# Performance work log

Hardware: AMD Instinct MI355X
Metric: run time of the kernel (lower is better)

## Reference

```python
import jax, jax.numpy as jnp
import numpy as np

EPS = 1e-6  # ieps_ln_default

def layernorm(x, g, b, ndims):
    # LayerNorm over the last `ndims` dims (matches nn.LayerNorm(normalized_shape))
    ax = tuple(range(x.ndim - ndims, x.ndim))
    m = jnp.mean(x, ax, keepdims=True)
    v = jnp.var(x, ax, keepdims=True)
    return (x - m) * jax.lax.rsqrt(v + EPS) * g + b

def setup_inputs() -> dict:
    key = jax.random.key(0)
    ks = jax.random.split(key, 9)
    B, S, H, D = 4, 2048, 8, 128   # bsize, seql, num_head, head_dim (isize=1024)
    FH = 512                        # _head_fhsize = 4*isize // num_head
    sc = 0.02
    return {
        "heads_input": jax.random.normal(ks[0], (B, S, H, D), jnp.float32),
        # trans_ifg: GroupLinear(2*hsize -> 2*hsize) per head
        "W_ifg": jax.random.normal(ks[1], (H, 2 * D, 2 * D), jnp.float32) * sc,
        "b_ifg": jnp.zeros((H, 2 * D), jnp.float32),
        # trans_hid: GroupLinear(2*hsize -> fhsize), LN, ReLU, GroupLinear(fhsize -> hsize)
        "W_hid1": jax.random.normal(ks[2], (H, 2 * D, FH), jnp.float32) * sc,
        "b_hid1": jnp.zeros((H, FH), jnp.float32),
        "hid_g": jnp.ones((H, FH), jnp.float32),
        "hid_b": jnp.zeros((H, FH), jnp.float32),
        "W_hid2": jax.random.normal(ks[3], (H, FH, D), jnp.float32) * sc,
        "b_hid2": jnp.zeros((H, D), jnp.float32),
        # trans_og: GroupLinear(2*hsize -> hsize) + LN
        "W_og": jax.random.normal(ks[4], (H, 2 * D, D), jnp.float32) * sc,
        "b_og": jnp.zeros((H, D), jnp.float32),
        "og_g": jnp.ones((H, D), jnp.float32),
        "og_b": jnp.zeros((H, D), jnp.float32),
        # normer_csum LN((H, D)); normer_ifg LN((H, 2, D))
        "csum_g": jnp.ones((H, D), jnp.float32),
        "csum_b": jnp.zeros((H, D), jnp.float32),
        "ifg_g": jnp.ones((H, 2, D), jnp.float32),
        "ifg_b": jnp.zeros((H, 2, D), jnp.float32),
        "init_cx": jnp.zeros((1, H, D), jnp.float32),
    }

def reference(heads_input, W_ifg, b_ifg, W_hid1, b_hid1, hid_g, hid_b,
              W_hid2, b_hid2, W_og, b_og, og_g, og_b,
              csum_g, csum_b, ifg_g, ifg_b, init_cx):
    B, S, H, D = heads_input.shape
    # normer_csum(cumsum of right-shifted input)
    shifted = jnp.concatenate([jnp.zeros((B, 1, H, D), heads_input.dtype),
                               heads_input[:, :-1]], axis=1)
    csum = layernorm(jnp.cumsum(shifted, axis=1), csum_g, csum_b, 2)
    gh = jnp.concatenate([heads_input, csum], axis=-1)  # (B,S,H,2D)
    # input/forget gates: per-head GroupLinear then LN over (H,2,D)
    ifg = jnp.einsum('bshi,hio->bsho', gh, W_ifg) + b_ifg
    ifg = layernorm(ifg.reshape(B, S, H, 2, D), ifg_g, ifg_b, 3)
    igate, fgate = ifg[..., 0, :], ifg[..., 1, :]
    # hidden: GroupLinear -> LN -> ReLU -> GroupLinear
    hid = jnp.einsum('bshi,hio->bsho', gh, W_hid1) + b_hid1
    hid = jax.nn.relu(layernorm(hid, hid_g, hid_b, 2))
    hidden = jnp.einsum('bshi,hio->bsho', hid, W_hid2) + b_hid2
    fgate = jax.nn.sigmoid(fgate)
    igh = jax.nn.sigmoid(igate) * hidden
    # LGateFunc: cell_t = fgate_t * cell_{t-1} + igh_t, cell_0 from init_cx
    c0 = jnp.broadcast_to(init_cx, (B, H, D)).astype(heads_input.dtype)
    def step(c, x):
        f, i = x
        c = f * c + i
        return c, c
    _, cells = jax.lax.scan(step, c0, (jnp.moveaxis(fgate, 1, 0), jnp.moveaxis(igh, 1, 0)))
    cell = jnp.moveaxis(cells, 0, 1)  # (B,S,H,D)
    # output gate
    og = jnp.einsum('bshi,hio->bsho', jnp.concatenate([heads_input, cell], axis=-1), W_og) + b_og
    og = layernorm(og, og_g, og_b, 2)
    return jax.nn.sigmoid(og) * cell
```

## Files before the change

### kernel.cpp

```cpp
#include <hip/hip_runtime.h>
#include <hip/hip_bf16.h>

#define DEV static __device__ __forceinline__

constexpr int B = 4, S = 2048, H = 8, D = 128, FH = 512;
constexpr int M = B * S;
constexpr int SC = 64;
constexpr int NCH = S / SC;

typedef __attribute__((ext_vector_type(8))) short short8;
typedef __attribute__((ext_vector_type(4))) float f32x4;

DEV float sigmoidf_(float x) { return 1.0f / (1.0f + __expf(-x)); }
DEV float b2f(unsigned short u) { union { unsigned int i; float f; } x; x.i = (unsigned int)u << 16; return x.f; }
DEV unsigned short f2bu(float f) { __hip_bfloat16 b = __float2bfloat16(f); union { __hip_bfloat16 b; unsigned short u; } x; x.b = b; return x.u; }

__global__ void k_wcvt(const float* __restrict__ W, __hip_bfloat16* __restrict__ Wt,
                       int K, int N) {
  __shared__ float t[32][33];
  int h = blockIdx.z;
  int k0 = blockIdx.x * 32, n0 = blockIdx.y * 32;
  int tx = threadIdx.x, ty = threadIdx.y;
  #pragma unroll
  for (int r = 0; r < 32; r += 8)
    t[ty + r][tx] = W[((size_t)h * K + k0 + ty + r) * N + n0 + tx];
  __syncthreads();
  #pragma unroll
  for (int r = 0; r < 32; r += 8)
    Wt[((size_t)h * N + n0 + ty + r) * K + k0 + tx] = __float2bfloat16(t[tx][ty + r]);
}

__global__ void k_pre1(const float* __restrict__ x, float* __restrict__ chsum) {
  int bh = blockIdx.x, ch = blockIdx.y, d = threadIdx.x;
  int b = bh >> 3, h = bh & 7;
  size_t base = ((size_t)(b * S + ch * SC) * H + h) * D + d;
  float s = 0.0f;
  for (int i = 0; i < SC; ++i) s += x[base + (size_t)i * H * D];
  chsum[((size_t)bh * NCH + ch) * D + d] = s;
}

__global__ void k_pre2(const float* __restrict__ chsum, float* __restrict__ choff) {
  int bh = blockIdx.x, d = threadIdx.x;
  float a = 0.0f;
  for (int c = 0; c < NCH; ++c) {
    size_t idx = ((size_t)bh * NCH + c) * D + d;
    choff[idx] = a;
    a += chsum[idx];
  }
}

__global__ void k_pre3(const float* __restrict__ x, const float* __restrict__ choff,
                       __hip_bfloat16* __restrict__ P) {
  int bh = blockIdx.x, ch = blockIdx.y, d = threadIdx.x;
  int b = bh >> 3, h = bh & 7;
  float acc = choff[((size_t)bh * NCH + ch) * D + d];
  for (int i = 0; i < SC; ++i) {
    size_t mh = ((size_t)b * S + ch * SC + i) * H + h;
    P[mh * D + d] = __float2bfloat16(acc);
    acc += x[mh * D + d];
  }
}

DEV void block_stats(float lsum, float lss, int n, float& mean, float& var) {
  #pragma unroll
  for (int o = 32; o > 0; o >>= 1) {
    lsum += __shfl_down(lsum, o);
    lss  += __shfl_down(lss, o);
  }
  __shared__ float wsum[4], wss[4];
  int wid = threadIdx.x >> 6;
  if ((threadIdx.x & 63) == 0) { wsum[wid] = lsum; wss[wid] = lss; }
  __syncthreads();
  float s = 0.0f, q = 0.0f;
  #pragma unroll
  for (int i = 0; i < 4; ++i) { s += wsum[i]; q += wss[i]; }
  mean = s / n;
  var = q / n - mean * mean;
}

__global__ __launch_bounds__(256) void k_csum_ln(const __hip_bfloat16* __restrict__ P,
                                                 const float* __restrict__ g,
                                                 const float* __restrict__ bb,
                                                 __hip_bfloat16* __restrict__ csum) {
  size_t m = blockIdx.x;
  int t = threadIdx.x;
  ushort4 raw = ((const ushort4*)(P + m * 1024))[t];
  float v0 = b2f(raw.x), v1 = b2f(raw.y), v2 = b2f(raw.z), v3 = b2f(raw.w);
  float lsum = v0 + v1 + v2 + v3;
  float lss = v0 * v0 + v1 * v1 + v2 * v2 + v3 * v3;
  float mean, var;
  block_stats(lsum, lss, 1024, mean, var);
  float rs = rsqrtf(var + 1e-6f);
  float4 gv = *(const float4*)(g + t * 4);
  float4 bv = *(const float4*)(bb + t * 4);
  ushort4 o;
  o.x = f2bu((v0 - mean) * rs * gv.x + bv.x);
  o.y = f2bu((v1 - mean) * rs * gv.y + bv.y);
  o.z = f2bu((v2 - mean) * rs * gv.z + bv.z);
  o.w = f2bu((v3 - mean) * rs * gv.w + bv.w);
  ((ushort4*)((unsigned short*)csum + m * 1024))[t] = o;
}

template <int N, int K, int AKIND, int EPI>
__global__ __launch_bounds__(512) void k_mgemm(
    const __hip_bfloat16* __restrict__ Ab,
    const float* __restrict__ Af0, const float* __restrict__ Af1,
    const __hip_bfloat16* __restrict__ Wt, const float* __restrict__ bias,
    float* __restrict__ out_f, __hip_bfloat16* __restrict__ out_b,
    float* __restrict__ ifg) {
  constexpr int BM = 256, BN = 128, BK = 32;
  constexpr int LDA = 40;
  __shared__ __align__(16) short As[BM * LDA];
  __shared__ __align__(16) short Bs[BN * LDA];
  int h = blockIdx.z;
  int m0 = blockIdx.y * BM, n0 = blockIdx.x * BN;
  int tid = threadIdx.x;
  int w = tid >> 6, lane = tid & 63;
  int wr = w >> 1, wc = w & 1;
  int l15 = lane & 15, l4 = lane >> 4;
  f32x4 acc[4][4] = {};
  for (int kt = 0; kt < K; kt += BK) {
    #pragma unroll
    for (int r = 0; r < 2; ++r) {
      int q = tid + r * 512;
      int row = q >> 2, cq = q & 3;
      int kk = kt + cq * 8;
      short8 v;
      if (AKIND == 0) {
        v = *reinterpret_cast<const short8*>(Ab + ((size_t)(m0 + row) * H + h) * K + kk);
      } else if (AKIND == 2 && kk >= D) {
        v = *reinterpret_cast<const short8*>(Ab + ((size_t)(m0 + row) * H + h) * D + (kk - D));
      } else {
        const float* src;
        if (AKIND == 1 && kk >= D) src = Af1 + ((size_t)(m0 + row) * H + h) * D + (kk - D);
        else                       src = Af0 + ((size_t)(m0 + row) * H + h) * D + kk;
        float4 f0 = ((const float4*)src)[0];
        float4 f1 = ((const float4*)src)[1];
        short8 t;
        t[0] = (short)f2bu(f0.x); t[1] = (short)f2bu(f0.y);
        t[2] = (short)f2bu(f0.z); t[3] = (short)f2bu(f0.w);
        t[4] = (short)f2bu(f1.x); t[5] = (short)f2bu(f1.y);
        t[6] = (short)f2bu(f1.z); t[7] = (short)f2bu(f1.w);
        v = t;
      }
      *reinterpret_cast<short8*>(As + row * LDA + cq * 8) = v;
    }
    {
      int row = tid >> 2, cq = tid & 3;
      short8 v = *reinterpret_cast<const short8*>(
          Wt + ((size_t)h * N + n0 + row) * K + kt + cq * 8);
      *reinterpret_cast<short8*>(Bs + row * LDA + cq * 8) = v;
    }
    __syncthreads();
    short8 a[4], bfr[4];
    #pragma unroll
    for (int i = 0; i < 4; ++i)
      a[i] = *reinterpret_cast<const short8*>(As + (wr * 64 + i * 16 + l15) * LDA + l4 * 8);
    #pragma unroll
    for (int j = 0; j < 4; ++j)
      bfr[j] = *reinterpret_cast<const short8*>(Bs + (wc * 64 + j * 16 + l15) * LDA + l4 * 8);
    #pragma unroll
    for (int i = 0; i < 4; ++i)
      #pragma unroll
      for (int j = 0; j < 4; ++j)
        acc[i][j] = __builtin_amdgcn_mfma_f32_16x16x32_bf16(a[i], bfr[j], acc[i][j], 0, 0, 0);
    __syncthreads();
  }
  #pragma unroll
  for (int i = 0; i < 4; ++i) {
    #pragma unroll
    for (int j = 0; j < 4; ++j) {
      #pragma unroll
      for (int r = 0; r < 4; ++r) {
        int mg = m0 + wr * 64 + i * 16 + l4 * 4 + r;
        int o = n0 + wc * 64 + j * 16 + l15;
        float v = acc[i][j][r] + bias[h * N + o];
        size_t mh = (size_t)mg * H + h;
        if (EPI == 0) {
          out_f[mh * N + o] = v;
        } else if (EPI == 1) {
          out_b[mh * N + o] = __float2bfloat16(v);
        } else {
          size_t idx = mh * 256 + o;
          ifg[idx] = ifg[idx] * v;
        }
      }
    }
  }
}

__global__ __launch_bounds__(256) void k_ifg_ln(float* __restrict__ ifg,
                                                const float* __restrict__ g,
                                                const float* __restrict__ bb) {
  size_t m = blockIdx.x;
  float* row = ifg + m * 2048;
  int t = threadIdx.x;
  float4 v0 = ((const float4*)row)[t];
  float4 v1 = ((const float4*)row)[t + 256];
  float lsum = v0.x + v0.y + v0.z + v0.w + v1.x + v1.y + v1.z + v1.w;
  float lss = v0.x * v0.x + v0.y * v0.y + v0.z * v0.z + v0.w * v0.w +
              v1.x * v1.x + v1.y * v1.y + v1.z * v1.z + v1.w * v1.w;
  float mean, var;
  block_stats(lsum, lss, 2048, mean, var);
  float rs = rsqrtf(var + 1e-6f);
  float4 g0 = ((const float4*)g)[t], g1 = ((const float4*)g)[t + 256];
  float4 b0 = ((const float4*)bb)[t], b1 = ((const float4*)bb)[t + 256];
  float4 o0, o1;
  o0.x = sigmoidf_((v0.x - mean) * rs * g0.x + b0.x);
  o0.y = sigmoidf_((v0.y - mean) * rs * g0.y + b0.y);
  o0.z = sigmoidf_((v0.z - mean) * rs * g0.z + b0.z);
  o0.w = sigmoidf_((v0.w - mean) * rs * g0.w + b0.w);
  o1.x = sigmoidf_((v1.x - mean) * rs * g1.x + b1.x);
  o1.y = sigmoidf_((v1.y - mean) * rs * g1.y + b1.y);
  o1.z = sigmoidf_((v1.z - mean) * rs * g1.z + b1.z);
  o1.w = sigmoidf_((v1.w - mean) * rs * g1.w + b1.w);
  ((float4*)row)[t] = o0;
  ((float4*)row)[t + 256] = o1;
}

__global__ __launch_bounds__(256) void k_hid_ln(__hip_bfloat16* __restrict__ hid,
                                                const float* __restrict__ g,
                                                const float* __restrict__ bb) {
  size_t m = blockIdx.x;
  unsigned short* row = (unsigned short*)(hid + m * 4096);
  int t = threadIdx.x;
  short8 r0 = ((const short8*)row)[t * 2];
  short8 r1 = ((const short8*)row)[t * 2 + 1];
  float v[16];
  float lsum = 0.0f, lss = 0.0f;
  #pragma unroll
  for (int i = 0; i < 8; ++i) {
    v[i] = b2f((unsigned short)r0[i]);
    v[i + 8] = b2f((unsigned short)r1[i]);
  }
  #pragma unroll
  for (int i = 0; i < 16; ++i) { lsum += v[i]; lss += v[i] * v[i]; }
  float mean, var;
  block_stats(lsum, lss, 4096, mean, var);
  float rs = rsqrtf(var + 1e-6f);
  short8 o0, o1;
  #pragma unroll
  for (int i = 0; i < 16; ++i) {
    int j = t * 16 + i;
    float o = (v[i] - mean) * rs * g[j] + bb[j];
    o = o > 0.0f ? o : 0.0f;
    if (i < 8) o0[i] = (short)f2bu(o); else o1[i - 8] = (short)f2bu(o);
  }
  ((short8*)row)[t * 2] = o0;
  ((short8*)row)[t * 2 + 1] = o1;
}

__global__ void k_scan1(const float* __restrict__ ifg, float* __restrict__ chF,
                        float* __restrict__ chI) {
  int bh = blockIdx.x, ch = blockIdx.y, d = threadIdx.x;
  int b = bh >> 3, h = bh & 7;
  float F = 1.0f, I = 0.0f;
  for (int i = 0; i < SC; ++i) {
    size_t mh = ((size_t)b * S + ch * SC + i) * H + h;
    float iv = ifg[mh * 256 + d];
    float fv = ifg[mh * 256 + 128 + d];
    F *= fv;
    I = fv * I + iv;
  }
  size_t idx = ((size_t)bh * NCH + ch) * D + d;
  chF[idx] = F;
  chI[idx] = I;
}

__global__ void k_scan2(const float* __restrict__ chF, const float* __restrict__ chI,
                        const float* __restrict__ init_cx, float* __restrict__ cst) {
  int bh = blockIdx.x, d = threadIdx.x;
  int h = bh & 7;
  float c = init_cx[h * D + d];
  for (int ch = 0; ch < NCH; ++ch) {
    size_t idx = ((size_t)bh * NCH + ch) * D + d;
    cst[idx] = c;
    c = chF[idx] * c + chI[idx];
  }
}

__global__ void k_scan3(const float* __restrict__ ifg, const float* __restrict__ cst,
                        float* __restrict__ cell) {
  int bh = blockIdx.x, ch = blockIdx.y, d = threadIdx.x;
  int b = bh >> 3, h = bh & 7;
  float c = cst[((size_t)bh * NCH + ch) * D + d];
  for (int i = 0; i < SC; ++i) {
    size_t mh = ((size_t)b * S + ch * SC + i) * H + h;
    c = ifg[mh * 256 + 128 + d] * c + ifg[mh * 256 + d];
    cell[mh * D + d] = c;
  }
}

__global__ __launch_bounds__(256) void k_og_out(const float* __restrict__ og,
                                                const float* __restrict__ cell,
                                                const float* __restrict__ g,
                                                const float* __restrict__ bb,
                                                float* __restrict__ out) {
  size_t m = blockIdx.x;
  const float* row = og + m * 1024;
  int t = threadIdx.x;
  float4 v = ((const float4*)row)[t];
  float lsum = v.x + v.y + v.z + v.w;
  float lss = v.x * v.x + v.y * v.y + v.z * v.z + v.w * v.w;
  float mean, var;
  block_stats(lsum, lss, 1024, mean, var);
  float rs = rsqrtf(var + 1e-6f);
  float4 gv = ((const float4*)g)[t];
  float4 bv = ((const float4*)bb)[t];
  float4 cv = ((const float4*)(cell + m * 1024))[t];
  float4 o;
  o.x = sigmoidf_((v.x - mean) * rs * gv.x + bv.x) * cv.x;
  o.y = sigmoidf_((v.y - mean) * rs * gv.y + bv.y) * cv.y;
  o.z = sigmoidf_((v.z - mean) * rs * gv.z + bv.z) * cv.z;
  o.w = sigmoidf_((v.w - mean) * rs * gv.w + bv.w) * cv.w;
  ((float4*)(out + m * 1024))[t] = o;
}

extern "C" void kernel_launch(void* const* d_in, const int* in_sizes, int n_in,
                              void* d_out, int out_size, void* d_ws, size_t ws_size,
                              hipStream_t stream) {
  (void)in_sizes; (void)n_in; (void)out_size; (void)ws_size;
  const float* x       = (const float*)d_in[0];
  const float* W_ifg   = (const float*)d_in[1];
  const float* b_ifg   = (const float*)d_in[2];
  const float* W_hid1  = (const float*)d_in[3];
  const float* b_hid1  = (const float*)d_in[4];
  const float* hid_g   = (const float*)d_in[5];
  const float* hid_b   = (const float*)d_in[6];
  const float* W_hid2  = (const float*)d_in[7];
  const float* b_hid2  = (const float*)d_in[8];
  const float* W_og    = (const float*)d_in[9];
  const float* b_og    = (const float*)d_in[10];
  const float* og_g    = (const float*)d_in[11];
  const float* og_b    = (const float*)d_in[12];
  const float* csum_g  = (const float*)d_in[13];
  const float* csum_b  = (const float*)d_in[14];
  const float* ifg_g   = (const float*)d_in[15];
  const float* ifg_b   = (const float*)d_in[16];
  const float* init_cx = (const float*)d_in[17];
  float* out = (float*)d_out;

  char* w = (char*)d_ws;
  __hip_bfloat16* Pb     = (__hip_bfloat16*)w;
  float* ifg             = (float*)w;
  float* og              = (float*)w;
  __hip_bfloat16* hid    = (__hip_bfloat16*)(w + 67108864);
  float* cell            = (float*)(w + 67108864);
  __hip_bfloat16* csum   = (__hip_bfloat16*)(w + 134217728);
  __hip_bfloat16* wt_ifg = (__hip_bfloat16*)(w + 150994944);
  __hip_bfloat16* wt_h1  = (__hip_bfloat16*)(w + 152043520);
  __hip_bfloat16* wt_h2  = (__hip_bfloat16*)(w + 154140672);
  __hip_bfloat16* wt_og  = (__hip_bfloat16*)(w + 155189248);
  float* chsum           = (float*)(w + 155713536);
  float* choff           = (float*)(w + 156237824);
  float* chF             = (float*)(w + 156762112);
  float* chI             = (float*)(w + 157286400);
  float* cst             = (float*)(w + 157810688);

  k_wcvt<<<dim3(8, 8, 8),  dim3(32, 8), 0, stream>>>(W_ifg,  wt_ifg, 256, 256);
  k_wcvt<<<dim3(8, 16, 8), dim3(32, 8), 0, stream>>>(W_hid1, wt_h1,  256, 512);
  k_wcvt<<<dim3(16, 4, 8), dim3(32, 8), 0, stream>>>(W_hid2, wt_h2,  512, 128);
  k_wcvt<<<dim3(8, 4, 8),  dim3(32, 8), 0, stream>>>(W_og,   wt_og,  256, 128);

  k_pre1<<<dim3(32, NCH), dim3(D), 0, stream>>>(x, chsum);
  k_pre2<<<dim3(32), dim3(D), 0, stream>>>(chsum, choff);
  k_pre3<<<dim3(32, NCH), dim3(D), 0, stream>>>(x, choff, Pb);
  k_csum_ln<<<dim3(M), dim3(256), 0, stream>>>(Pb, csum_g, csum_b, csum);

  k_mgemm<256, 256, 2, 0><<<dim3(2, 32, 8), dim3(512), 0, stream>>>(
      csum, x, nullptr, wt_ifg, b_ifg, ifg, nullptr, nullptr);
  k_mgemm<512, 256, 2, 1><<<dim3(4, 32, 8), dim3(512), 0, stream>>>(
      csum, x, nullptr, wt_h1, b_hid1, nullptr, hid, nullptr);

  k_ifg_ln<<<dim3(M), dim3(256), 0, stream>>>(ifg, ifg_g, ifg_b);
  k_hid_ln<<<dim3(M), dim3(256), 0, stream>>>(hid, hid_g, hid_b);
  k_mgemm<128, 512, 0, 2><<<dim3(1, 32, 8), dim3(512), 0, stream>>>(
      hid, nullptr, nullptr, wt_h2, b_hid2, nullptr, nullptr, ifg);

  k_scan1<<<dim3(32, NCH), dim3(D), 0, stream>>>(ifg, chF, chI);
  k_scan2<<<dim3(32), dim3(D), 0, stream>>>(chF, chI, init_cx, cst);
  k_scan3<<<dim3(32, NCH), dim3(D), 0, stream>>>(ifg, cst, cell);

  k_mgemm<128, 256, 1, 0><<<dim3(1, 32, 8), dim3(512), 0, stream>>>(
      nullptr, x, cell, wt_og, b_og, og, nullptr, nullptr);
  k_og_out<<<dim3(M), dim3(256), 0, stream>>>(og, cell, og_g, og_b, out);
}
```

Baseline: 371.7 us.

## Fuse layernorms into GEMM prologue/epilogue and store intermediates as bf16

Removes the standalone ifg and hidden layernorm kernels. Row statistics are now accumulated with atomics in the GEMM epilogues, and normalization plus ReLU or sigmoid is applied on the fly in the consuming GEMM prologue and epilogue and in the scan kernels. Intermediates (gh concat, ifg, hid, og, cell) are stored as bf16 instead of fp32. Block indices are remapped and M-tiles are halved for the smaller GEMMs to raise the block count. This cuts global memory traffic and kernel launches, but adds atomics, recomputed sigmoids and some precision loss.

```diff
diff --git a/kernel.cpp b/kernel.cpp
--- a/kernel.cpp
+++ b/kernel.cpp
@@ -14,6 +14,10 @@
 DEV float sigmoidf_(float x) { return 1.0f / (1.0f + __expf(-x)); }
 DEV float b2f(unsigned short u) { union { unsigned int i; float f; } x; x.i = (unsigned int)u << 16; return x.f; }
 DEV unsigned short f2bu(float f) { __hip_bfloat16 b = __float2bfloat16(f); union { __hip_bfloat16 b; unsigned short u; } x; x.b = b; return x.u; }
+
+__global__ void k_zero(float4* __restrict__ p) {
+  p[blockIdx.x * 256 + threadIdx.x] = float4{0.f, 0.f, 0.f, 0.f};
+}
 
 __global__ void k_wcvt(const float* __restrict__ W, __hip_bfloat16* __restrict__ Wt,
                        int K, int N) {
@@ -30,12 +34,17 @@
     Wt[((size_t)h * N + n0 + ty + r) * K + k0 + tx] = __float2bfloat16(t[tx][ty + r]);
 }
 
-__global__ void k_pre1(const float* __restrict__ x, float* __restrict__ chsum) {
+__global__ void k_pre1(const float* __restrict__ x, float* __restrict__ chsum,
+                       unsigned short* __restrict__ gh) {
   int bh = blockIdx.x, ch = blockIdx.y, d = threadIdx.x;
   int b = bh >> 3, h = bh & 7;
-  size_t base = ((size_t)(b * S + ch * SC) * H + h) * D + d;
   float s = 0.0f;
-  for (int i = 0; i < SC; ++i) s += x[base + (size_t)i * H * D];
+  for (int i = 0; i < SC; ++i) {
+    size_t mh = ((size_t)(b * S + ch * SC + i) * H + h);
+    float xv = x[mh * D + d];
+    gh[mh * 256 + d] = f2bu(xv);
+    s += xv;
+  }
   chsum[((size_t)bh * NCH + ch) * D + d] = s;
 }
 
@@ -49,15 +58,16 @@
   }
 }
 
-__global__ void k_pre3(const float* __restrict__ x, const float* __restrict__ choff,
+__global__ void k_pre3(const unsigned short* __restrict__ gh,
+                       const float* __restrict__ choff,
                        __hip_bfloat16* __restrict__ P) {
   int bh = blockIdx.x, ch = blockIdx.y, d = threadIdx.x;
   int b = bh >> 3, h = bh & 7;
   float acc = choff[((size_t)bh * NCH + ch) * D + d];
   for (int i = 0; i < SC; ++i) {
-    size_t mh = ((size_t)b * S + ch * SC + i) * H + h;
+    size_t mh = ((size_t)(b * S + ch * SC + i) * H + h);
     P[mh * D + d] = __float2bfloat16(acc);
-    acc += x[mh * D + d];
+    acc += b2f(gh[mh * 256 + d]);
   }
 }
 
@@ -81,7 +91,7 @@
 __global__ __launch_bounds__(256) void k_csum_ln(const __hip_bfloat16* __restrict__ P,
                                                  const float* __restrict__ g,
                                                  const float* __restrict__ bb,
-                                                 __hip_bfloat16* __restrict__ csum) {
+                                                 unsigned short* __restrict__ gh) {
   size_t m = blockIdx.x;
   int t = threadIdx.x;
   ushort4 raw = ((const ushort4*)(P + m * 1024))[t];
@@ -93,55 +103,80 @@
   float rs = rsqrtf(var + 1e-6f);
   float4 gv = *(const float4*)(g + t * 4);
   float4 bv = *(const float4*)(bb + t * 4);
+  int h = t >> 5;
+  int d0 = (t * 4) & 127;
   ushort4 o;
   o.x = f2bu((v0 - mean) * rs * gv.x + bv.x);
   o.y = f2bu((v1 - mean) * rs * gv.y + bv.y);
   o.z = f2bu((v2 - mean) * rs * gv.z + bv.z);
   o.w = f2bu((v3 - mean) * rs * gv.w + bv.w);
-  ((ushort4*)((unsigned short*)csum + m * 1024))[t] = o;
-}
-
-template <int N, int K, int AKIND, int EPI>
+  *(ushort4*)(gh + (m * 8 + h) * 256 + 128 + d0) = o;
+}
+
+__global__ void k_finalize(const float* __restrict__ isum, const float* __restrict__ iss,
+                           const float* __restrict__ hsum, const float* __restrict__ hss,
+                           float2* __restrict__ ims, float2* __restrict__ hms) {
+  int m = blockIdx.x * 256 + threadIdx.x;
+  float mean = isum[m] / 2048.0f;
+  float var = iss[m] / 2048.0f - mean * mean;
+  ims[m] = float2{mean, rsqrtf(var + 1e-6f)};
+  mean = hsum[m] / 4096.0f;
+  var = hss[m] / 4096.0f - mean * mean;
+  hms[m] = float2{mean, rsqrtf(var + 1e-6f)};
+}
+
+template <int BM_, int N, int K, int AKIND, int EPI, bool STATS>
 __global__ __launch_bounds__(512) void k_mgemm(
-    const __hip_bfloat16* __restrict__ Ab,
-    const float* __restrict__ Af0, const float* __restrict__ Af1,
+    const __hip_bfloat16* __restrict__ Ab, const __hip_bfloat16* __restrict__ Ab2,
+    const float2* __restrict__ Ams, const float* __restrict__ Ag,
+    const float* __restrict__ Abeta,
     const __hip_bfloat16* __restrict__ Wt, const float* __restrict__ bias,
-    float* __restrict__ out_f, __hip_bfloat16* __restrict__ out_b,
-    float* __restrict__ ifg) {
-  constexpr int BM = 256, BN = 128, BK = 32;
+    __hip_bfloat16* __restrict__ out_b,
+    const __hip_bfloat16* __restrict__ ifg_raw, const float2* __restrict__ ifg_ms,
+    const float* __restrict__ ifg_gw, const float* __restrict__ ifg_bw,
+    __hip_bfloat16* __restrict__ igh,
+    float* __restrict__ st_sum, float* __restrict__ st_ss) {
+  constexpr int BN = 128, BK = 32;
   constexpr int LDA = 40;
-  __shared__ __align__(16) short As[BM * LDA];
+  constexpr int MT = M / BM_;
+  constexpr int NT = N / BN;
+  constexpr int MI = BM_ / 64;
+  __shared__ __align__(16) short As[BM_ * LDA];
   __shared__ __align__(16) short Bs[BN * LDA];
-  int h = blockIdx.z;
-  int m0 = blockIdx.y * BM, n0 = blockIdx.x * BN;
+  int bid = blockIdx.x;
+  int r = bid & 7, q = bid >> 3;
+  int p = q / NT, n = q % NT;
+  int mh = r * MT + p;
+  int m0 = (mh >> 3) * BM_;
+  int h = mh & 7;
+  int n0 = n * BN;
   int tid = threadIdx.x;
   int w = tid >> 6, lane = tid & 63;
   int wr = w >> 1, wc = w & 1;
   int l15 = lane & 15, l4 = lane >> 4;
-  f32x4 acc[4][4] = {};
+  f32x4 acc[MI][4] = {};
   for (int kt = 0; kt < K; kt += BK) {
     #pragma unroll
-    for (int r = 0; r < 2; ++r) {
-      int q = tid + r * 512;
-      int row = q >> 2, cq = q & 3;
+    for (int rr = 0; rr < BM_ / 128; ++rr) {
+      int qq = tid + rr * 512;
+      int row = qq >> 2, cq = qq & 3;
       int kk = kt + cq * 8;
+      int mg = m0 + row;
       short8 v;
       if (AKIND == 0) {
-        v = *reinterpret_cast<const short8*>(Ab + ((size_t)(m0 + row) * H + h) * K + kk);
-      } else if (AKIND == 2 && kk >= D) {
-        v = *reinterpret_cast<const short8*>(Ab + ((size_t)(m0 + row) * H + h) * D + (kk - D));
+        v = *reinterpret_cast<const short8*>(Ab + ((size_t)mg * H + h) * K + kk);
+      } else if (AKIND == 2) {
+        if (kk < 128) v = *reinterpret_cast<const short8*>(Ab + ((size_t)mg * H + h) * 256 + kk);
+        else          v = *reinterpret_cast<const short8*>(Ab2 + ((size_t)mg * H + h) * 128 + kk - 128);
       } else {
-        const float* src;
-        if (AKIND == 1 && kk >= D) src = Af1 + ((size_t)(m0 + row) * H + h) * D + (kk - D);
-        else                       src = Af0 + ((size_t)(m0 + row) * H + h) * D + kk;
-        float4 f0 = ((const float4*)src)[0];
-        float4 f1 = ((const float4*)src)[1];
-        short8 t;
-        t[0] = (short)f2bu(f0.x); t[1] = (short)f2bu(f0.y);
-        t[2] = (short)f2bu(f0.z); t[3] = (short)f2bu(f0.w);
-        t[4] = (short)f2bu(f1.x); t[5] = (short)f2bu(f1.y);
-        t[6] = (short)f2bu(f1.z); t[7] = (short)f2bu(f1.w);
-        v = t;
+        short8 t0 = *reinterpret_cast<const short8*>(Ab + ((size_t)mg * H + h) * K + kk);
+        float2 ms = Ams[mg];
+        #pragma unroll
+        for (int e = 0; e < 8; ++e) {
+          float f = (b2f((unsigned short)t0[e]) - ms.x) * ms.y * Ag[h * K + kk + e]
+                    + Abeta[h * K + kk + e];
+          v[e] = (short)f2bu(f > 0.0f ? f : 0.0f);
+        }
       }
       *reinterpret_cast<short8*>(As + row * LDA + cq * 8) = v;
     }
@@ -152,119 +187,78 @@
       *reinterpret_cast<short8*>(Bs + row * LDA + cq * 8) = v;
     }
     __syncthreads();
-    short8 a[4], bfr[4];
+    short8 a[MI], bfr[4];
     #pragma unroll
-    for (int i = 0; i < 4; ++i)
-      a[i] = *reinterpret_cast<const short8*>(As + (wr * 64 + i * 16 + l15) * LDA + l4 * 8);
+    for (int i = 0; i < MI; ++i)
+      a[i] = *reinterpret_cast<const short8*>(As + (wr * (MI * 16) + i * 16 + l15) * LDA + l4 * 8);
     #pragma unroll
     for (int j = 0; j < 4; ++j)
       bfr[j] = *reinterpret_cast<const short8*>(Bs + (wc * 64 + j * 16 + l15) * LDA + l4 * 8);
     #pragma unroll
-    for (int i = 0; i < 4; ++i)
+    for (int i = 0; i < MI; ++i)
       #pragma unroll
       for (int j = 0; j < 4; ++j)
         acc[i][j] = __builtin_amdgcn_mfma_f32_16x16x32_bf16(a[i], bfr[j], acc[i][j], 0, 0, 0);
     __syncthreads();
   }
   #pragma unroll
-  for (int i = 0; i < 4; ++i) {
+  for (int i = 0; i < MI; ++i) {
     #pragma unroll
-    for (int j = 0; j < 4; ++j) {
+    for (int rr2 = 0; rr2 < 4; ++rr2) {
+      int mg = m0 + wr * (MI * 16) + i * 16 + l4 * 4 + rr2;
+      size_t mhn = (size_t)mg * H + h;
+      float lsum = 0.0f, lss = 0.0f;
       #pragma unroll
-      for (int r = 0; r < 4; ++r) {
-        int mg = m0 + wr * 64 + i * 16 + l4 * 4 + r;
+      for (int j = 0; j < 4; ++j) {
         int o = n0 + wc * 64 + j * 16 + l15;
-        float v = acc[i][j][r] + bias[h * N + o];
-        size_t mh = (size_t)mg * H + h;
+        float v = acc[i][j][rr2] + bias[h * N + o];
         if (EPI == 0) {
-          out_f[mh * N + o] = v;
-        } else if (EPI == 1) {
-          out_b[mh * N + o] = __float2bfloat16(v);
+          out_b[mhn * N + o] = __float2bfloat16(v);
         } else {
-          size_t idx = mh * 256 + o;
-          ifg[idx] = ifg[idx] * v;
+          float ig = b2f(*(const unsigned short*)(ifg_raw + mhn * 256 + o));
+          float2 ms = ifg_ms[mg];
+          float gi = sigmoidf_((ig - ms.x) * ms.y * ifg_gw[h * 256 + o] + ifg_bw[h * 256 + o]);
+          igh[mhn * 128 + o] = __float2bfloat16(gi * v);
+        }
+        lsum += v; lss += v * v;
+      }
+      if constexpr (STATS) {
+        #pragma unroll
+        for (int ox = 8; ox > 0; ox >>= 1) {
+          lsum += __shfl_xor(lsum, ox);
+          lss  += __shfl_xor(lss, ox);
+        }
+        if (l15 == 0) {
+          atomicAdd(&st_sum[mg], lsum);
+          atomicAdd(&st_ss[mg], lss);
         }
       }
     }
   }
 }
 
-__global__ __launch_bounds__(256) void k_ifg_ln(float* __restrict__ ifg,
-                                                const float* __restrict__ g,
-                                                const float* __restrict__ bb) {
-  size_t m = blockIdx.x;
-  float* row = ifg + m * 2048;
-  int t = threadIdx.x;
-  float4 v0 = ((const float4*)row)[t];
-  float4 v1 = ((const float4*)row)[t + 256];
-  float lsum = v0.x + v0.y + v0.z + v0.w + v1.x + v1.y + v1.z + v1.w;
-  float lss = v0.x * v0.x + v0.y * v0.y + v0.z * v0.z + v0.w * v0.w +
-              v1.x * v1.x + v1.y * v1.y + v1.z * v1.z + v1.w * v1.w;
-  float mean, var;
-  block_stats(lsum, lss, 2048, mean, var);
-  float rs = rsqrtf(var + 1e-6f);
-  float4 g0 = ((const float4*)g)[t], g1 = ((const float4*)g)[t + 256];
-  float4 b0 = ((const float4*)bb)[t], b1 = ((const float4*)bb)[t + 256];
-  float4 o0, o1;
-  o0.x = sigmoidf_((v0.x - mean) * rs * g0.x + b0.x);
-  o0.y = sigmoidf_((v0.y - mean) * rs * g0.y + b0.y);
-  o0.z = sigmoidf_((v0.z - mean) * rs * g0.z + b0.z);
-  o0.w = sigmoidf_((v0.w - mean) * rs * g0.w + b0.w);
-  o1.x = sigmoidf_((v1.x - mean) * rs * g1.x + b1.x);
-  o1.y = sigmoidf_((v1.y - mean) * rs * g1.y + b1.y);
-  o1.z = sigmoidf_((v1.z - mean) * rs * g1.z + b1.z);
-  o1.w = sigmoidf_((v1.w - mean) * rs * g1.w + b1.w);
-  ((float4*)row)[t] = o0;
-  ((float4*)row)[t + 256] = o1;
-}
-
-__global__ __launch_bounds__(256) void k_hid_ln(__hip_bfloat16* __restrict__ hid,
-                                                const float* __restrict__ g,
-                                                const float* __restrict__ bb) {
-  size_t m = blockIdx.x;
-  unsigned short* row = (unsigned short*)(hid + m * 4096);
-  int t = threadIdx.x;
-  short8 r0 = ((const short8*)row)[t * 2];
-  short8 r1 = ((const short8*)row)[t * 2 + 1];
-  float v[16];
-  float lsum = 0.0f, lss = 0.0f;
-  #pragma unroll
-  for (int i = 0; i < 8; ++i) {
-    v[i] = b2f((unsigned short)r0[i]);
-    v[i + 8] = b2f((unsigned short)r1[i]);
-  }
-  #pragma unroll
-  for (int i = 0; i < 16; ++i) { lsum += v[i]; lss += v[i] * v[i]; }
-  float mean, var;
-  block_stats(lsum, lss, 4096, mean, var);
-  float rs = rsqrtf(var + 1e-6f);
-  short8 o0, o1;
-  #pragma unroll
-  for (int i = 0; i < 16; ++i) {
-    int j = t * 16 + i;
-    float o = (v[i] - mean) * rs * g[j] + bb[j];
-    o = o > 0.0f ? o : 0.0f;
-    if (i < 8) o0[i] = (short)f2bu(o); else o1[i - 8] = (short)f2bu(o);
-  }
-  ((short8*)row)[t * 2] = o0;
-  ((short8*)row)[t * 2 + 1] = o1;
-}
-
-__global__ void k_scan1(const float* __restrict__ ifg, float* __restrict__ chF,
-                        float* __restrict__ chI) {
+__global__ void k_scan1(const __hip_bfloat16* __restrict__ ifg_raw,
+                        const float2* __restrict__ ms_arr,
+                        const float* __restrict__ ifg_gw, const float* __restrict__ ifg_bw,
+                        const __hip_bfloat16* __restrict__ igh,
+                        float* __restrict__ chF, float* __restrict__ chI) {
   int bh = blockIdx.x, ch = blockIdx.y, d = threadIdx.x;
   int b = bh >> 3, h = bh & 7;
-  float F = 1.0f, I = 0.0f;
+  float gw = ifg_gw[h * 256 + 128 + d], gb = ifg_bw[h * 256 + 128 + d];
+  float F = 1.0f, Iv = 0.0f;
+  int mb = b * S + ch * SC;
   for (int i = 0; i < SC; ++i) {
-    size_t mh = ((size_t)b * S + ch * SC + i) * H + h;
-    float iv = ifg[mh * 256 + d];
-    float fv = ifg[mh * 256 + 128 + d];
-    F *= fv;
-    I = fv * I + iv;
+    int m = mb + i;
+    size_t mh = (size_t)m * H + h;
+    float2 ms = ms_arr[m];
+    float f = sigmoidf_((b2f(*(const unsigned short*)(ifg_raw + mh * 256 + 128 + d)) - ms.x) * ms.y * gw + gb);
+    float iv = b2f(*(const unsigned short*)(igh + mh * 128 + d));
+    F *= f;
+    Iv = f * Iv + iv;
   }
   size_t idx = ((size_t)bh * NCH + ch) * D + d;
   chF[idx] = F;
-  chI[idx] = I;
+  chI[idx] = Iv;
 }
 
 __global__ void k_scan2(const float* __restrict__ chF, const float* __restrict__ chI,
@@ -279,40 +273,50 @@
   }
 }
 
-__global__ void k_scan3(const float* __restrict__ ifg, const float* __restrict__ cst,
-                        float* __restrict__ cell) {
+__global__ void k_scan3(const __hip_bfloat16* __restrict__ ifg_raw,
+                        const float2* __restrict__ ms_arr,
+                        const float* __restrict__ ifg_gw, const float* __restrict__ ifg_bw,
+                        const __hip_bfloat16* __restrict__ igh,
+                        const float* __restrict__ cst,
+                        __hip_bfloat16* __restrict__ cell) {
   int bh = blockIdx.x, ch = blockIdx.y, d = threadIdx.x;
   int b = bh >> 3, h = bh & 7;
+  float gw = ifg_gw[h * 256 + 128 + d], gb = ifg_bw[h * 256 + 128 + d];
   float c = cst[((size_t)bh * NCH + ch) * D + d];
+  int mb = b * S + ch * SC;
   for (int i = 0; i < SC; ++i) {
-    size_t mh = ((size_t)b * S + ch * SC + i) * H + h;
-    c = ifg[mh * 256 + 128 + d] * c + ifg[mh * 256 + d];
-    cell[mh * D + d] = c;
-  }
-}
-
-__global__ __launch_bounds__(256) void k_og_out(const float* __restrict__ og,
-                                                const float* __restrict__ cell,
+    int m = mb + i;
+    size_t mh = (size_t)m * H + h;
+    float2 ms = ms_arr[m];
+    float f = sigmoidf_((b2f(*(const unsigned short*)(ifg_raw + mh * 256 + 128 + d)) - ms.x) * ms.y * gw + gb);
+    float iv = b2f(*(const unsigned short*)(igh + mh * 128 + d));
+    c = f * c + iv;
+    cell[mh * 128 + d] = __float2bfloat16(c);
+  }
+}
+
+__global__ __launch_bounds__(256) void k_og_out(const __hip_bfloat16* __restrict__ og,
+                                                const __hip_bfloat16* __restrict__ cell,
                                                 const float* __restrict__ g,
                                                 const float* __restrict__ bb,
                                                 float* __restrict__ out) {
   size_t m = blockIdx.x;
-  const float* row = og + m * 1024;
   int t = threadIdx.x;
-  float4 v = ((const float4*)row)[t];
-  float lsum = v.x + v.y + v.z + v.w;
-  float lss = v.x * v.x + v.y * v.y + v.z * v.z + v.w * v.w;
+  ushort4 raw = ((const ushort4*)(og + m * 1024))[t];
+  float v0 = b2f(raw.x), v1 = b2f(raw.y), v2 = b2f(raw.z), v3 = b2f(raw.w);
+  float lsum = v0 + v1 + v2 + v3;
+  float lss = v0 * v0 + v1 * v1 + v2 * v2 + v3 * v3;
   float mean, var;
   block_stats(lsum, lss, 1024, mean, var);
   float rs = rsqrtf(var + 1e-6f);
-  float4 gv = ((const float4*)g)[t];
-  float4 bv = ((const float4*)bb)[t];
-  float4 cv = ((const float4*)(cell + m * 1024))[t];
+  float4 gv = *(const float4*)(g + t * 4);
+  float4 bv = *(const float4*)(bb + t * 4);
+  ushort4 cv = ((const ushort4*)(cell + m * 1024))[t];
   float4 o;
-  o.x = sigmoidf_((v.x - mean) * rs * gv.x + bv.x) * cv.x;
-  o.y = sigmoidf_((v.y - mean) * rs * gv.y + bv.y) * cv.y;
-  o.z = sigmoidf_((v.z - mean) * rs * gv.z + bv.z) * cv.z;
-  o.w = sigmoidf_((v.w - mean) * rs * gv.w + bv.w) * cv.w;
+  o.x = sigmoidf_((v0 - mean) * rs * gv.x + bv.x) * b2f(cv.x);
+  o.y = sigmoidf_((v1 - mean) * rs * gv.y + bv.y) * b2f(cv.y);
+  o.z = sigmoidf_((v2 - mean) * rs * gv.z + bv.z) * b2f(cv.z);
+  o.w = sigmoidf_((v3 - mean) * rs * gv.w + bv.w) * b2f(cv.w);
   ((float4*)(out + m * 1024))[t] = o;
 }
 
@@ -341,47 +345,62 @@
   float* out = (float*)d_out;
 
   char* w = (char*)d_ws;
-  __hip_bfloat16* Pb     = (__hip_bfloat16*)w;
-  float* ifg             = (float*)w;
-  float* og              = (float*)w;
+  unsigned short* gh     = (unsigned short*)w;
+  __hip_bfloat16* ghb    = (__hip_bfloat16*)w;
+  __hip_bfloat16* ifg    = (__hip_bfloat16*)(w + 33554432);
+  __hip_bfloat16* og     = (__hip_bfloat16*)(w + 33554432);
   __hip_bfloat16* hid    = (__hip_bfloat16*)(w + 67108864);
-  float* cell            = (float*)(w + 67108864);
-  __hip_bfloat16* csum   = (__hip_bfloat16*)(w + 134217728);
+  __hip_bfloat16* cell   = (__hip_bfloat16*)(w + 67108864);
+  __hip_bfloat16* Pb     = (__hip_bfloat16*)(w + 134217728);
+  __hip_bfloat16* igh    = (__hip_bfloat16*)(w + 134217728);
   __hip_bfloat16* wt_ifg = (__hip_bfloat16*)(w + 150994944);
   __hip_bfloat16* wt_h1  = (__hip_bfloat16*)(w + 152043520);
   __hip_bfloat16* wt_h2  = (__hip_bfloat16*)(w + 154140672);
   __hip_bfloat16* wt_og  = (__hip_bfloat16*)(w + 155189248);
   float* chsum           = (float*)(w + 155713536);
   float* choff           = (float*)(w + 156237824);
-  float* chF             = (float*)(w + 156762112);
-  float* chI             = (float*)(w + 157286400);
-  float* cst             = (float*)(w + 157810688);
+  float* cst             = (float*)(w + 156762112);
+  float* ifg_sum         = (float*)(w + 157286400);
+  float* ifg_ss          = (float*)(w + 157319168);
+  float* hid_sum         = (float*)(w + 157351936);
+  float* hid_ss          = (float*)(w + 157384704);
+  float2* ifg_ms         = (float2*)(w + 157417472);
+  float2* hid_ms         = (float2*)(w + 157483008);
+  float* chF = chsum;
+  float* chI = choff;
+
+  k_zero<<<dim3(32), dim3(256), 0, stream>>>((float4*)ifg_sum);
 
   k_wcvt<<<dim3(8, 8, 8),  dim3(32, 8), 0, stream>>>(W_ifg,  wt_ifg, 256, 256);
   k_wcvt<<<dim3(8, 16, 8), dim3(32, 8), 0, stream>>>(W_hid1, wt_h1,  256, 512);
   k_wcvt<<<dim3(16, 4, 8), dim3(32, 8), 0, stream>>>(W_hid2, wt_h2,  512, 128);
   k_wcvt<<<dim3(8, 4, 8),  dim3(32, 8), 0, stream>>>(W_og,   wt_og,  256, 128);
 
-  k_pre1<<<dim3(32, NCH), dim3(D), 0, stream>>>(x, chsum);
+  k_pre1<<<dim3(32, NCH), dim3(D), 0, stream>>>(x, chsum, gh);
   k_pre2<<<dim3(32), dim3(D), 0, stream>>>(chsum, choff);
-  k_pre3<<<dim3(32, NCH), dim3(D), 0, stream>>>(x, choff, Pb);
-  k_csum_ln<<<dim3(M), dim3(256), 0, stream>>>(Pb, csum_g, csum_b, csum);
-
-  k_mgemm<256, 256, 2, 0><<<dim3(2, 32, 8), dim3(512), 0, stream>>>(
-      csum, x, nullptr, wt_ifg, b_ifg, ifg, nullptr, nullptr);
-  k_mgemm<512, 256, 2, 1><<<dim3(4, 32, 8), dim3(512), 0, stream>>>(
-      csum, x, nullptr, wt_h1, b_hid1, nullptr, hid, nullptr);
-
-  k_ifg_ln<<<dim3(M), dim3(256), 0, stream>>>(ifg, ifg_g, ifg_b);
-  k_hid_ln<<<dim3(M), dim3(256), 0, stream>>>(hid, hid_g, hid_b);
-  k_mgemm<128, 512, 0, 2><<<dim3(1, 32, 8), dim3(512), 0, stream>>>(
-      hid, nullptr, nullptr, wt_h2, b_hid2, nullptr, nullptr, ifg);
-
-  k_scan1<<<dim3(32, NCH), dim3(D), 0, stream>>>(ifg, chF, chI);
+  k_pre3<<<dim3(32, NCH), dim3(D), 0, stream>>>(gh, choff, Pb);
+  k_csum_ln<<<dim3(M), dim3(256), 0, stream>>>(Pb, csum_g, csum_b, gh);
+
+  k_mgemm<256, 256, 256, 0, 0, true><<<dim3(512), dim3(512), 0, stream>>>(
+      ghb, nullptr, nullptr, nullptr, nullptr, wt_ifg, b_ifg, ifg,
+      nullptr, nullptr, nullptr, nullptr, nullptr, ifg_sum, ifg_ss);
+  k_mgemm<256, 512, 256, 0, 0, true><<<dim3(1024), dim3(512), 0, stream>>>(
+      ghb, nullptr, nullptr, nullptr, nullptr, wt_h1, b_hid1, hid,
+      nullptr, nullptr, nullptr, nullptr, nullptr, hid_sum, hid_ss);
+
+  k_finalize<<<dim3(32), dim3(256), 0, stream>>>(
+      ifg_sum, ifg_ss, hid_sum, hid_ss, ifg_ms, hid_ms);
+
+  k_mgemm<128, 128, 512, 1, 2, false><<<dim3(512), dim3(512), 0, stream>>>(
+      hid, nullptr, hid_ms, hid_g, hid_b, wt_h2, b_hid2, nullptr,
+      ifg, ifg_ms, ifg_g, ifg_b, igh, nullptr, nullptr);
+
+  k_scan1<<<dim3(32, NCH), dim3(D), 0, stream>>>(ifg, ifg_ms, ifg_g, ifg_b, igh, chF, chI);
   k_scan2<<<dim3(32), dim3(D), 0, stream>>>(chF, chI, init_cx, cst);
-  k_scan3<<<dim3(32, NCH), dim3(D), 0, stream>>>(ifg, cst, cell);
-
-  k_mgemm<128, 256, 1, 0><<<dim3(1, 32, 8), dim3(512), 0, stream>>>(
-      nullptr, x, cell, wt_og, b_og, og, nullptr, nullptr);
+  k_scan3<<<dim3(32, NCH), dim3(D), 0, stream>>>(ifg, ifg_ms, ifg_g, ifg_b, igh, cst, cell);
+
+  k_mgemm<128, 128, 256, 2, 0, false><<<dim3(512), dim3(512), 0, stream>>>(
+      ghb, cell, nullptr, nullptr, nullptr, wt_og, b_og, og,
+      nullptr, nullptr, nullptr, nullptr, nullptr, nullptr, nullptr);
   k_og_out<<<dim3(M), dim3(256), 0, stream>>>(og, cell, og_g, og_b, out);
 }
```

After: 384.5 us. 3.4% more time.
